# Kernel tuning notes

Hardware: AMD Instinct MI355X
Metric: run time of the kernel (lower is better)

The kernel has to match this reference:

```python
import jax, jax.numpy as jnp
import numpy as np

B, T, F = 2048, 336, 10
H1, H2, D1, D2 = 70, 21, 30, 20


def _lstm_dir(xg, w_hh):
    """Run one LSTM direction. xg: [T, B, 4H] = x@W_ih^T + b_ih + b_hh (precomputed).
    Gate order matches PyTorch: i, f, g, o."""
    H = w_hh.shape[1]
    h0 = jnp.zeros((xg.shape[1], H), xg.dtype)

    def step(carry, g_in):
        h, c = carry
        g = g_in + h @ w_hh.T
        i, f, gg, o = jnp.split(g, 4, axis=-1)
        c = jax.nn.sigmoid(f) * c + jax.nn.sigmoid(i) * jnp.tanh(gg)
        h = jax.nn.sigmoid(o) * jnp.tanh(c)
        return (h, c), h

    _, hs = jax.lax.scan(step, (h0, h0), xg)
    return hs  # [T, B, H]


def _bilstm(x, wf_ih, wf_hh, bf_ih, bf_hh, wb_ih, wb_hh, bb_ih, bb_hh):
    """Bidirectional LSTM, batch_first in/out. x: [B, T, I] -> [B, T, 2H]."""
    xt = x.transpose(1, 0, 2)  # [T, B, I]
    gf = xt @ wf_ih.T + (bf_ih + bf_hh)
    hf = _lstm_dir(gf, wf_hh)
    gb = (xt @ wb_ih.T + (bb_ih + bb_hh))[::-1]
    hb = _lstm_dir(gb, wb_hh)[::-1]
    return jnp.concatenate([hf, hb], axis=-1).transpose(1, 0, 2)


def setup_inputs() -> dict:
    key = jax.random.key(0)
    ks = iter(jax.random.split(key, 32))

    def u(shape, h):  # PyTorch default init: U(-1/sqrt(H), 1/sqrt(H))
        s = 1.0 / np.sqrt(h)
        return jax.random.uniform(next(ks), shape, jnp.float32, -s, s)

    inp = {"x": jax.random.normal(next(ks), (B, T, F), jnp.float32)}
    # lstm1: input F, hidden H1, bidirectional
    for d in ("f", "b"):
        inp[f"w1{d}_ih"] = u((4 * H1, F), H1)
        inp[f"w1{d}_hh"] = u((4 * H1, H1), H1)
        inp[f"b1{d}_ih"] = u((4 * H1,), H1)
        inp[f"b1{d}_hh"] = u((4 * H1,), H1)
    # lstm2: input 2*H1, hidden H2, bidirectional
    for d in ("f", "b"):
        inp[f"w2{d}_ih"] = u((4 * H2, 2 * H1), H2)
        inp[f"w2{d}_hh"] = u((4 * H2, H2), H2)
        inp[f"b2{d}_ih"] = u((4 * H2,), H2)
        inp[f"b2{d}_hh"] = u((4 * H2,), H2)
    # dense head
    inp["wd1"] = u((D1, 2 * H2), 2 * H2)
    inp["bd1"] = u((D1,), 2 * H2)
    inp["wd2"] = u((D2, D1), D1)
    inp["bd2"] = u((D2,), D1)
    inp["wo"] = u((1, D2), D2)
    inp["bo"] = u((1,), D2)
    return inp


def reference(x,
              w1f_ih, w1f_hh, b1f_ih, b1f_hh, w1b_ih, w1b_hh, b1b_ih, b1b_hh,
              w2f_ih, w2f_hh, b2f_ih, b2f_hh, w2b_ih, w2b_hh, b2b_ih, b2b_hh,
              wd1, bd1, wd2, bd2, wo, bo):
    h = _bilstm(x, w1f_ih, w1f_hh, b1f_ih, b1f_hh, w1b_ih, w1b_hh, b1b_ih, b1b_hh)
    h = _bilstm(h, w2f_ih, w2f_hh, b2f_ih, b2f_hh, w2b_ih, w2b_hh, b2b_ih, b2b_hh)
    h = jax.nn.relu(h @ wd1.T + bd1)
    h = jax.nn.relu(h @ wd2.T + bd2)
    return h @ wo.T + bo  # [B, T, 1]
```

## Files before the change

kernel.cpp:

```cpp
#include <hip/hip_runtime.h>

#define Bz 2048
#define Tz 336
#define Fz 10
#define H1 70
#define H2 21

typedef __attribute__((ext_vector_type(8))) short short8;
typedef __attribute__((ext_vector_type(4))) float float4v;

#define MFMA16(a, b, c) __builtin_amdgcn_mfma_f32_16x16x32_bf16((a), (b), (c), 0, 0, 0)

__device__ __forceinline__ void sync_lds() {
    asm volatile("s_waitcnt lgkmcnt(0)\n\ts_barrier" ::: "memory");
}

__device__ __forceinline__ unsigned short f2bf(float v) {
    unsigned int u = __float_as_uint(v);
    u += 0x7FFFu + ((u >> 16) & 1u);
    return (unsigned short)(u >> 16);
}
__device__ __forceinline__ float bf2f(unsigned short s) {
    return __uint_as_float(((unsigned int)s) << 16);
}

__device__ __forceinline__ float lstm_gate_h(float gi, float gf, float gc,
                                             float go, float& cst) {
    float a  = __expf(-gf);
    float b  = __expf(-gi);
    float d  = __expf(2.0f * gc);
    float pa = 1.0f + a;
    float pb = 1.0f + b;
    float pd = d + 1.0f;
    float t1 = pb * pd;
    float num = fmaf(pa, d - 1.0f, cst * t1);
    float cn  = num / (pa * t1);
    float e2  = __expf(-go);
    float f2  = __expf(2.0f * cn);
    float h   = (f2 - 1.0f) / ((1.0f + e2) * (f2 + 1.0f));
    cst = cn;
    return h;
}

__device__ __forceinline__ int frag_off(int m, int k) {
    return (k >> 3) * 128 + m * 8 + (k & 7);
}

__global__ __launch_bounds__(1024, 4) void k_lstm1(
    const float* __restrict__ x,
    const float* __restrict__ wih_f, const float* __restrict__ whh_f,
    const float* __restrict__ bih_f, const float* __restrict__ bhh_f,
    const float* __restrict__ wih_b, const float* __restrict__ whh_b,
    const float* __restrict__ bih_b, const float* __restrict__ bhh_b,
    unsigned short* __restrict__ y1)
{
    __shared__ short hB_hi[2][1536];

    const int tb  = blockIdx.x & 127;
    const int dir = blockIdx.x >> 7;
    const int b0  = tb << 4;
    const float* wih = dir ? wih_b : wih_f;
    const float* whh = dir ? whh_b : whh_f;
    const float* bih = dir ? bih_b : bih_f;
    const float* bhh = dir ? bhh_b : bhh_f;

    const int tid  = threadIdx.x;
    const int wv   = tid >> 6;
    const int lane = tid & 63;
    const int n    = lane & 15;
    const int quad = lane >> 4;
    const int NT1  = (wv < 2) ? 2 : 1;

    short8 whi[2][3], wlo[2][3];
    const int g_ = n & 3;
#pragma unroll
    for (int tt = 0; tt < 2; ++tt) {
        if (tt < NT1) {
            const int p  = wv + 16 * tt;
            const int uu = 4 * p + (n >> 2);
#pragma unroll
            for (int q = 0; q < 3; ++q) {
#pragma unroll
                for (int j = 0; j < 8; ++j) {
                    int k = q * 32 + quad * 8 + j;
                    float v = 0.0f;
                    if (uu < H1) {
                        int row = g_ * H1 + uu;
                        if (k < H1)        v = whh[row * H1 + k];
                        else if (k < 80)   v = wih[row * Fz + (k - H1)];
                        else if (k == 80)  v = bih[row] + bhh[row];
                    }
                    unsigned short hi = f2bf(v);
                    unsigned short lo = f2bf(v - bf2f(hi));
                    whi[tt][q][j] = (short)hi;
                    wlo[tt][q][j] = (short)lo;
                }
            }
        }
    }

    for (int e = tid; e < 1536; e += 1024) {
        hB_hi[0][e] = 0; hB_hi[1][e] = 0;
    }
    __syncthreads();
    if (tid < 16) {
        int off = 1280 + tid * 8;
        hB_hi[0][off] = (short)0x3F80;
        hB_hi[1][off] = (short)0x3F80;
    }

    const int es = tid - 864;
    const bool stg = (es >= 0 && es < 160);
    int sm = 0, sf = 0;
    if (stg) { sm = es / Fz; sf = es % Fz; }

    const int tstep = dir ? -1 : 1;
    const int t0    = dir ? (Tz - 1) : 0;

    float xv = 0.0f;
    if (stg) {
        float v = x[((size_t)(b0 + sm) * Tz + t0) * Fz + sf];
        hB_hi[0][frag_off(sm, H1 + sf)] = (short)f2bf(v);
        xv = x[((size_t)(b0 + sm) * Tz + t0 + tstep) * Fz + sf];
    }
    const float* xp = x + ((size_t)(b0 + sm) * Tz + t0 + 2 * tstep) * Fz + sf;
    const ptrdiff_t xinc = (ptrdiff_t)tstep * Fz;
    unsigned short* ypB = y1 + (size_t)(t0 * 128 + tb) * 2304;
    const ptrdiff_t yinc = (ptrdiff_t)tstep * (128 * 2304);

    const int xoff = frag_off(sm, H1 + sf);
    int hoff[2], yoff[2];
#pragma unroll
    for (int tt = 0; tt < 2; ++tt) {
        const int u = 4 * (wv + 16 * tt) + quad;
        hoff[tt] = frag_off(n, u);
        const int K = 32 + dir * H1 + u;
        yoff[tt] = ((K >> 3) * 16 + n) * 8 + (K & 7) - 512;
    }

    float cst[2];
    cst[0] = 0.0f; cst[1] = 0.0f;

    auto body = [&](int step, const int pp) __attribute__((always_inline)) {
        sync_lds();

        if (stg && step + 1 < Tz) {
            hB_hi[pp ^ 1][xoff] = (short)f2bf(xv);
        }
        if (stg && step + 2 < Tz) {
            xv = *xp;
        }

        short8 bhi[3];
#pragma unroll
        for (int q = 0; q < 3; ++q)
            bhi[q] = *(const short8*)&hB_hi[pp][q * 512 + lane * 8];

        float4v acc[2];
#pragma unroll
        for (int tt = 0; tt < 2; ++tt) acc[tt] = (float4v){0.f, 0.f, 0.f, 0.f};
#pragma unroll
        for (int tt = 0; tt < 2; ++tt) {
            if (tt < NT1) {
                acc[tt] = MFMA16(whi[tt][0], bhi[0], acc[tt]);
                acc[tt] = MFMA16(wlo[tt][0], bhi[0], acc[tt]);
                acc[tt] = MFMA16(whi[tt][1], bhi[1], acc[tt]);
                acc[tt] = MFMA16(wlo[tt][1], bhi[1], acc[tt]);
                acc[tt] = MFMA16(whi[tt][2], bhi[2], acc[tt]);
                acc[tt] = MFMA16(wlo[tt][2], bhi[2], acc[tt]);
            }
        }

#pragma unroll
        for (int tt = 0; tt < 2; ++tt) {
            if (tt < NT1) {
                const int u = 4 * (wv + 16 * tt) + quad;
                if (u < H1) {
                    float h = lstm_gate_h(acc[tt][0], acc[tt][1],
                                          acc[tt][2], acc[tt][3], cst[tt]);
                    unsigned short hh = f2bf(h);
                    hB_hi[pp ^ 1][hoff[tt]] = (short)hh;
                    ypB[yoff[tt]] = hh;
                }
            }
        }
        xp  += xinc;
        ypB += yinc;
    };

    for (int step = 0; step < Tz; step += 2) {
        body(step, 0);
        body(step + 1, 1);
    }
}

__global__ __launch_bounds__(512, 2) void k_lstm2(
    const unsigned short* __restrict__ y1,
    const float* __restrict__ wih_f, const float* __restrict__ whh_f,
    const float* __restrict__ bih_f, const float* __restrict__ bhh_f,
    const float* __restrict__ wih_b, const float* __restrict__ whh_b,
    const float* __restrict__ bih_b, const float* __restrict__ bhh_b,
    unsigned short* __restrict__ y2)
{
    __shared__ short hB_hi[2][3072];

    const int tb  = blockIdx.x & 127;
    const int dir = blockIdx.x >> 7;
    const int b0  = tb << 4;
    const float* wih = dir ? wih_b : wih_f;
    const float* whh = dir ? whh_b : whh_f;
    const float* bih = dir ? bih_b : bih_f;
    const float* bhh = dir ? bhh_b : bhh_f;

    const int tid  = threadIdx.x;
    const int wv   = tid >> 6;
    const int lane = tid & 63;
    const int n    = lane & 15;
    const int quad = lane >> 4;
    const bool comp = (wv < 6);

    short8 whi[6], wlo0;
    const int g_ = n & 3;
    if (comp) {
        const int uu = 4 * wv + (n >> 2);
#pragma unroll
        for (int q = 0; q < 6; ++q) {
#pragma unroll
            for (int j = 0; j < 8; ++j) {
                int k = q * 32 + quad * 8 + j;
                float v = 0.0f;
                if (uu < H2) {
                    int row = g_ * H2 + uu;
                    if (k < H2)                   v = whh[row * H2 + k];
                    else if (k == 21)             v = bih[row] + bhh[row];
                    else if (k >= 32 && k < 172)  v = wih[row * 140 + (k - 32)];
                }
                unsigned short hi = f2bf(v);
                whi[q][j] = (short)hi;
                if (q == 0) wlo0[j] = (short)f2bf(v - bf2f(hi));
            }
        }
    }

    for (int e = tid; e < 3072; e += 512) { hB_hi[0][e] = 0; hB_hi[1][e] = 0; }
    __syncthreads();
    if (tid < 16) {
        int off = frag_off(tid, 21);
        hB_hi[0][off] = (short)0x3F80;
        hB_hi[1][off] = (short)0x3F80;
    }

    const int es = tid - 224;
    const bool stg = (es >= 0 && es < 288);
    const bool hole = (es >= 272);

    const int tstep = dir ? -1 : 1;
    const int t0    = dir ? (Tz - 1) : 0;

    short8 xr = (short8){0,0,0,0,0,0,0,0};
    if (stg) {
        short8 v = *(const short8*)(y1 + ((size_t)t0 * 128 + tb) * 2304 + es * 8);
        if (hole) { v[4] = 0; v[5] = 0; v[6] = 0; v[7] = 0; }
        *(short8*)&hB_hi[0][512 + es * 8] = v;
        xr = *(const short8*)(y1 + ((size_t)(t0 + tstep) * 128 + tb) * 2304 + es * 8);
    }
    const unsigned short* srcp =
        y1 + ((size_t)(t0 + 2 * tstep) * 128 + tb) * 2304 + es * 8;
    const ptrdiff_t sinc = (ptrdiff_t)tstep * (128 * 2304);
    unsigned short* yp2 = y2 + ((size_t)(b0 + n) * Tz + t0) * 42 + dir * H2;
    const ptrdiff_t yinc = (ptrdiff_t)tstep * 42;

    const int u     = 4 * wv + quad;
    const int hoffc = frag_off(n, (u < H2) ? u : 0);

    float cst = 0.0f;

    auto body = [&](int step, const int pp) __attribute__((always_inline)) {
        sync_lds();

        if (stg && step + 1 < Tz) {
            short8 v = xr;
            if (hole) { v[4] = 0; v[5] = 0; v[6] = 0; v[7] = 0; }
            *(short8*)&hB_hi[pp ^ 1][512 + es * 8] = v;
        }
        if (stg && step + 2 < Tz) {
            xr = *(const short8*)srcp;
        }

        if (comp) {
            short8 bhi[6];
#pragma unroll
            for (int q = 0; q < 6; ++q)
                bhi[q] = *(const short8*)&hB_hi[pp][q * 512 + lane * 8];

            float4v acc = (float4v){0.f, 0.f, 0.f, 0.f};
            acc = MFMA16(whi[0], bhi[0], acc);
            acc = MFMA16(wlo0,   bhi[0], acc);
            acc = MFMA16(whi[1], bhi[1], acc);
            acc = MFMA16(whi[2], bhi[2], acc);
            acc = MFMA16(whi[3], bhi[3], acc);
            acc = MFMA16(whi[4], bhi[4], acc);
            acc = MFMA16(whi[5], bhi[5], acc);

            if (u < H2) {
                float h = lstm_gate_h(acc[0], acc[1], acc[2], acc[3], cst);
                unsigned short hh = f2bf(h);
                hB_hi[pp ^ 1][hoffc] = (short)hh;
                yp2[u] = hh;
            }
        }
        srcp += sinc;
        yp2  += yinc;
    };

    for (int step = 0; step < Tz; step += 2) {
        body(step, 0);
        body(step + 1, 1);
    }
}

__global__ __launch_bounds__(256) void k_dense(
    const unsigned short* __restrict__ y2,
    const float* __restrict__ wd1, const float* __restrict__ bd1,
    const float* __restrict__ wd2, const float* __restrict__ bd2,
    const float* __restrict__ wo,  const float* __restrict__ bo,
    float* __restrict__ out)
{
    int idx = blockIdx.x * 256 + threadIdx.x;
    if (idx >= Bz * Tz) return;
    const unsigned int* row = (const unsigned int*)&y2[(size_t)idx * 42];

    float v[42];
#pragma unroll
    for (int j = 0; j < 21; ++j) {
        unsigned int p = row[j];
        v[2 * j]     = bf2f((unsigned short)(p & 0xFFFFu));
        v[2 * j + 1] = bf2f((unsigned short)(p >> 16));
    }

    float h1[30];
#pragma unroll
    for (int o = 0; o < 30; ++o) {
        float s = bd1[o];
#pragma unroll
        for (int j = 0; j < 42; ++j) s = fmaf(v[j], wd1[o * 42 + j], s);
        h1[o] = fmaxf(s, 0.0f);
    }
    float outv = bo[0];
#pragma unroll
    for (int o = 0; o < 20; ++o) {
        float s = bd2[o];
#pragma unroll
        for (int j = 0; j < 30; ++j) s = fmaf(h1[j], wd2[o * 30 + j], s);
        outv = fmaf(fmaxf(s, 0.0f), wo[o], outv);
    }
    out[idx] = outv;
}

extern "C" void kernel_launch(void* const* d_in, const int* in_sizes, int n_in,
                              void* d_out, int out_size, void* d_ws, size_t ws_size,
                              hipStream_t stream)
{
    const float* x      = (const float*)d_in[0];
    const float* w1f_ih = (const float*)d_in[1];
    const float* w1f_hh = (const float*)d_in[2];
    const float* b1f_ih = (const float*)d_in[3];
    const float* b1f_hh = (const float*)d_in[4];
    const float* w1b_ih = (const float*)d_in[5];
    const float* w1b_hh = (const float*)d_in[6];
    const float* b1b_ih = (const float*)d_in[7];
    const float* b1b_hh = (const float*)d_in[8];
    const float* w2f_ih = (const float*)d_in[9];
    const float* w2f_hh = (const float*)d_in[10];
    const float* b2f_ih = (const float*)d_in[11];
    const float* b2f_hh = (const float*)d_in[12];
    const float* w2b_ih = (const float*)d_in[13];
    const float* w2b_hh = (const float*)d_in[14];
    const float* b2b_ih = (const float*)d_in[15];
    const float* b2b_hh = (const float*)d_in[16];
    const float* wd1    = (const float*)d_in[17];
    const float* bd1    = (const float*)d_in[18];
    const float* wd2    = (const float*)d_in[19];
    const float* bd2    = (const float*)d_in[20];
    const float* wo     = (const float*)d_in[21];
    const float* bo     = (const float*)d_in[22];
    float* out = (float*)d_out;

    const size_t y1_elems = (size_t)Tz * 128 * 2304;
    const size_t y2_elems = (size_t)Bz * Tz * 42;
    if (ws_size < (y1_elems + y2_elems) * 2) return;

    unsigned short* y1 = (unsigned short*)d_ws;
    unsigned short* y2 = y1 + y1_elems;

    hipLaunchKernelGGL(k_lstm1, dim3(256), dim3(1024), 0, stream,
                       x, w1f_ih, w1f_hh, b1f_ih, b1f_hh,
                       w1b_ih, w1b_hh, b1b_ih, b1b_hh, y1);
    hipLaunchKernelGGL(k_lstm2, dim3(256), dim3(512), 0, stream,
                       y1, w2f_ih, w2f_hh, b2f_ih, b2f_hh,
                       w2b_ih, w2b_hh, b2b_ih, b2b_hh, y2);
    hipLaunchKernelGGL(k_dense, dim3((Bz * Tz + 255) / 256), dim3(256), 0, stream,
                       y2, wd1, bd1, wd2, bd2, wo, bo, out);
}
```

Measured before the change: 574.4 us.

## Load LSTM2 input fragments directly into registers instead of staging via LDS

The second LSTM kernel no longer uses two staging waves that copy the y1 input slice into shared memory each step. Each compute wave now loads its five input MFMA B-fragments straight from global memory into double-buffered registers, masking the padded tail in registers. Only the 16x32 recurrent hidden fragment stays in LDS. The block shrinks to 384 threads and the input-projection MFMAs are issued before the LDS read of h, shortening the per-step serial path. The cost is redundant global loads across the six waves and more registers per thread.

After: 584.3 us. Within noise of the previous version (+1.7%).

```diff
diff --git a/kernel.cpp b/kernel.cpp
--- a/kernel.cpp
+++ b/kernel.cpp
@@ -194,7 +194,7 @@
     }
 }
 
-__global__ __launch_bounds__(512, 2) void k_lstm2(
+__global__ __launch_bounds__(384, 2) void k_lstm2(
     const unsigned short* __restrict__ y1,
     const float* __restrict__ wih_f, const float* __restrict__ whh_f,
     const float* __restrict__ bih_f, const float* __restrict__ bhh_f,
@@ -202,7 +202,7 @@
     const float* __restrict__ bih_b, const float* __restrict__ bhh_b,
     unsigned short* __restrict__ y2)
 {
-    __shared__ short hB_hi[2][3072];
+    __shared__ short hH[2][512];
 
     const int tb  = blockIdx.x & 127;
     const int dir = blockIdx.x >> 7;
@@ -217,11 +217,10 @@
     const int lane = tid & 63;
     const int n    = lane & 15;
     const int quad = lane >> 4;
-    const bool comp = (wv < 6);
 
     short8 whi[6], wlo0;
     const int g_ = n & 3;
-    if (comp) {
+    {
         const int uu = 4 * wv + (n >> 2);
 #pragma unroll
         for (int q = 0; q < 6; ++q) {
@@ -242,30 +241,37 @@
         }
     }
 
-    for (int e = tid; e < 3072; e += 512) { hB_hi[0][e] = 0; hB_hi[1][e] = 0; }
+    unsigned int kmask[4];
+#pragma unroll
+    for (int w2 = 0; w2 < 4; ++w2) {
+        unsigned int m0 = (quad * 8 + 2 * w2     >= 12) ? 0u : 0xFFFFu;
+        unsigned int m1 = (quad * 8 + 2 * w2 + 1 >= 12) ? 0u : 0xFFFFu;
+        kmask[w2] = m0 | (m1 << 16);
+    }
+
+    for (int e = tid; e < 512; e += 384) { hH[0][e] = 0; hH[1][e] = 0; }
     __syncthreads();
     if (tid < 16) {
         int off = frag_off(tid, 21);
-        hB_hi[0][off] = (short)0x3F80;
-        hB_hi[1][off] = (short)0x3F80;
-    }
-
-    const int es = tid - 224;
-    const bool stg = (es >= 0 && es < 288);
-    const bool hole = (es >= 272);
+        hH[0][off] = (short)0x3F80;
+        hH[1][off] = (short)0x3F80;
+    }
 
     const int tstep = dir ? -1 : 1;
     const int t0    = dir ? (Tz - 1) : 0;
 
-    short8 xr = (short8){0,0,0,0,0,0,0,0};
-    if (stg) {
-        short8 v = *(const short8*)(y1 + ((size_t)t0 * 128 + tb) * 2304 + es * 8);
-        if (hole) { v[4] = 0; v[5] = 0; v[6] = 0; v[7] = 0; }
-        *(short8*)&hB_hi[0][512 + es * 8] = v;
-        xr = *(const short8*)(y1 + ((size_t)(t0 + tstep) * 128 + tb) * 2304 + es * 8);
+    short8 xg0[5], xg1[5];
+    {
+        const unsigned short* r0p = y1 + ((size_t)t0 * 128 + tb) * 2304 + lane * 8;
+        const unsigned short* r1p = y1 + ((size_t)(t0 + tstep) * 128 + tb) * 2304 + lane * 8;
+#pragma unroll
+        for (int q = 0; q < 5; ++q) {
+            xg0[q] = *(const short8*)(r0p + q * 512);
+            xg1[q] = *(const short8*)(r1p + q * 512);
+        }
     }
     const unsigned short* srcp =
-        y1 + ((size_t)(t0 + 2 * tstep) * 128 + tb) * 2304 + es * 8;
+        y1 + ((size_t)(t0 + 2 * tstep) * 128 + tb) * 2304 + lane * 8;
     const ptrdiff_t sinc = (ptrdiff_t)tstep * (128 * 2304);
     unsigned short* yp2 = y2 + ((size_t)(b0 + n) * Tz + t0) * 42 + dir * H2;
     const ptrdiff_t yinc = (ptrdiff_t)tstep * 42;
@@ -275,47 +281,48 @@
 
     float cst = 0.0f;
 
-    auto body = [&](int step, const int pp) __attribute__((always_inline)) {
+    auto body = [&](int step, const int pp, short8 (&xg)[5])
+        __attribute__((always_inline)) {
         sync_lds();
 
-        if (stg && step + 1 < Tz) {
-            short8 v = xr;
-            if (hole) { v[4] = 0; v[5] = 0; v[6] = 0; v[7] = 0; }
-            *(short8*)&hB_hi[pp ^ 1][512 + es * 8] = v;
-        }
-        if (stg && step + 2 < Tz) {
-            xr = *(const short8*)srcp;
-        }
-
-        if (comp) {
-            short8 bhi[6];
-#pragma unroll
-            for (int q = 0; q < 6; ++q)
-                bhi[q] = *(const short8*)&hB_hi[pp][q * 512 + lane * 8];
-
-            float4v acc = (float4v){0.f, 0.f, 0.f, 0.f};
-            acc = MFMA16(whi[0], bhi[0], acc);
-            acc = MFMA16(wlo0,   bhi[0], acc);
-            acc = MFMA16(whi[1], bhi[1], acc);
-            acc = MFMA16(whi[2], bhi[2], acc);
-            acc = MFMA16(whi[3], bhi[3], acc);
-            acc = MFMA16(whi[4], bhi[4], acc);
-            acc = MFMA16(whi[5], bhi[5], acc);
-
-            if (u < H2) {
-                float h = lstm_gate_h(acc[0], acc[1], acc[2], acc[3], cst);
-                unsigned short hh = f2bf(h);
-                hB_hi[pp ^ 1][hoffc] = (short)hh;
-                yp2[u] = hh;
-            }
+        short8 bhi0 = *(const short8*)&hH[pp][lane * 8];
+
+        short8 x4 = xg[4];
+        {
+            unsigned int* xw = (unsigned int*)&x4;
+            xw[0] &= kmask[0]; xw[1] &= kmask[1];
+            xw[2] &= kmask[2]; xw[3] &= kmask[3];
+        }
+
+        float4v acc = (float4v){0.f, 0.f, 0.f, 0.f};
+        acc = MFMA16(whi[1], xg[0], acc);
+        acc = MFMA16(whi[2], xg[1], acc);
+        acc = MFMA16(whi[3], xg[2], acc);
+        acc = MFMA16(whi[4], xg[3], acc);
+        acc = MFMA16(whi[5], x4,    acc);
+
+        if (step + 2 < Tz) {
+#pragma unroll
+            for (int q = 0; q < 5; ++q)
+                xg[q] = *(const short8*)(srcp + q * 512);
+        }
+
+        acc = MFMA16(whi[0], bhi0, acc);
+        acc = MFMA16(wlo0,   bhi0, acc);
+
+        float h = lstm_gate_h(acc[0], acc[1], acc[2], acc[3], cst);
+        unsigned short hh = f2bf(h);
+        if (u < H2) {
+            hH[pp ^ 1][hoffc] = (short)hh;
+            yp2[u] = hh;
         }
         srcp += sinc;
         yp2  += yinc;
     };
 
     for (int step = 0; step < Tz; step += 2) {
-        body(step, 0);
-        body(step + 1, 1);
+        body(step,     0, xg0);
+        body(step + 1, 1, xg1);
     }
 }
 
@@ -396,7 +403,7 @@
     hipLaunchKernelGGL(k_lstm1, dim3(256), dim3(1024), 0, stream,
                        x, w1f_ih, w1f_hh, b1f_ih, b1f_hh,
                        w1b_ih, w1b_hh, b1b_ih, b1b_hh, y1);
-    hipLaunchKernelGGL(k_lstm2, dim3(256), dim3(512), 0, stream,
+    hipLaunchKernelGGL(k_lstm2, dim3(256), dim3(384), 0, stream,
                        y1, w2f_ih, w2f_hh, b2f_ih, b2f_hh,
                        w2b_ih, w2b_hh, b2b_ih, b2b_hh, y2);
     hipLaunchKernelGGL(k_dense, dim3((Bz * Tz + 255) / 256), dim3(256), 0, stream,
```
